# Kernel tuning notes

Measured on AMD Instinct MI355X. Metric: run time of the kernel, lower is better.

## Reference

```python
import jax, jax.numpy as jnp
import numpy as np

TAU = 2.0          # LIF membrane time constant (decay_input=True)
VTH = 1.0          # spiking threshold (hidden layers); last layer has inf threshold
EPS = 1e-5         # batchnorm eps
ALPHA = 2.0        # ATan surrogate-gradient alpha
HL = 8             # HLfreq_ratio (chunk length in timesteps)
SIZES = [1024, 1024, 512]

@jax.custom_vjp
def spike(x):
    return (x >= 0).astype(x.dtype)

def _spike_fwd(x):
    return (x >= 0).astype(x.dtype), x

def _spike_bwd(x, g):
    # spikingjelly ATan surrogate: alpha/2 / (1 + (pi/2 * alpha * x)^2)
    return (g * (ALPHA / 2.0) / (1.0 + (jnp.pi / 2.0 * ALPHA * x) ** 2),)

spike.defvjp(_spike_fwd, _spike_bwd)

def setup_inputs() -> dict:
    key = jax.random.key(0)
    ks = jax.random.split(key, 1 + len(SIZES))
    T, B, D = 1024, 32, 512
    inp = {"x": jax.random.normal(ks[0], (T, B, D), dtype=jnp.float32)}
    d_in = D
    for i, s in enumerate(SIZES):
        inp[f"W{i}"] = jax.random.normal(ks[i + 1], (s, d_in), dtype=jnp.float32) / np.float32(np.sqrt(d_in))
        inp[f"b{i}"] = jnp.zeros((s,), jnp.float32)
        inp[f"g{i}"] = jnp.ones((s,), jnp.float32)    # BN gamma
        inp[f"bt{i}"] = jnp.zeros((s,), jnp.float32)  # BN beta
        d_in = s
    return inp

def _forward(x, params):
    # x: [T, B, d_in]; process chunks of HL timesteps, membrane state carried across chunks
    n_chunks = x.shape[0] // HL
    B = x.shape[1]
    xr = x.reshape(n_chunks, HL, B, x.shape[2])
    n_layers = len(params)
    vs0 = tuple(jnp.zeros((B, p[0].shape[0]), x.dtype) for p in params)

    def chunk_step(vs, xc):  # xc: [HL, B, d_in]
        h = xc
        new_vs = []
        for i, (W, b, g, bt) in enumerate(params):
            # Linear over all timesteps of the chunk
            h = jnp.einsum('tbd,ed->tbe', h, W) + b
            # BatchNorm (training mode): stats over (time, batch) of this chunk, per channel
            mu = h.mean((0, 1))
            var = jnp.mean((h - mu) ** 2, (0, 1))
            h = g * (h - mu) * jax.lax.rsqrt(var + EPS) + bt
            last = (i == n_layers - 1)

            def step(v, xt, last=last):
                v = v + (xt - v) / TAU          # decay_input=True LIF charge
                if last:
                    return v, v                 # inf threshold: pure leaky integrator, emit v_seq
                s = spike(v - VTH)
                return v * (1.0 - s), s         # hard reset to v_reset=0

            v_new, h = jax.lax.scan(step, vs[i], h)
            new_vs.append(v_new)
        # reduction_mode='mean_mempot': mean of last layer's v_seq over chunk timesteps
        return tuple(new_vs), h.mean(0)

    _, z = jax.lax.scan(chunk_step, vs0, xr)
    return z  # [n_chunks, B, d_output]

def reference(x, W0, b0, g0, bt0, W1, b1, g1, bt1, W2, b2, g2, bt2):
    params = [(W0, b0, g0, bt0), (W1, b1, g1, bt1), (W2, b2, g2, bt2)]
    return _forward(x, params)
```

## Files before the change

kernel.cpp:

```cpp
#include <hip/hip_runtime.h>
#include <hip/hip_bf16.h>
#include <stdint.h>


__global__ void k_zero(unsigned int* __restrict__ p, int n){
  int i = blockIdx.x * 256 + threadIdx.x;
  if (i < n) p[i] = 0u;
}

__global__ void k_transpose(const float* __restrict__ in, float* __restrict__ out, int R, int C){
  __shared__ float tile[32][33];
  int bx = blockIdx.x * 32, by = blockIdx.y * 32;
  int tx = threadIdx.x, ty = threadIdx.y;
  for (int i = ty; i < 32; i += 8)
    tile[i][tx] = in[(size_t)(by + i) * C + bx + tx];
  __syncthreads();
  for (int i = ty; i < 32; i += 8)
    out[(size_t)(bx + i) * R + by + tx] = tile[tx][i];
}

__global__ __launch_bounds__(256, 3) void k_gemm_np(const float* __restrict__ A,
    const float* __restrict__ Bw, const float* __restrict__ bias,
    float* __restrict__ C, int M){
  (void)M;
  __shared__ float As[32][132];
  __shared__ float Bs[32][132];
  int bm = blockIdx.y * 128;
  int bn = blockIdx.x * 128;
  int tid = threadIdx.x;
  int kk = tid & 31, q = tid >> 5;
  int c = (tid & 7) | ((tid & 64) >> 3);
  int r = ((tid >> 3) & 7) | ((tid & 128) >> 4);
  int giA = (2 * r) ^ (r >> 2);
  int giB = (2 * c) ^ (c >> 2);
  float acc[8][8];
#pragma unroll
  for (int ii = 0; ii < 8; ++ii)
#pragma unroll
    for (int jj = 0; jj < 8; ++jj) acc[ii][jj] = 0.f;

  for (int k0 = 0; k0 < 512; k0 += 32){
#pragma unroll
    for (int rr = 0; rr < 4; ++rr){
      int colb = q * 4 + rr * 32;
      int gi = (colb >> 2) ^ (colb >> 5) ^ (kk >> 3);
      float4 va, vb;
      va.x = A[(size_t)(bm + colb + 0) * 512 + k0 + kk];
      va.y = A[(size_t)(bm + colb + 1) * 512 + k0 + kk];
      va.z = A[(size_t)(bm + colb + 2) * 512 + k0 + kk];
      va.w = A[(size_t)(bm + colb + 3) * 512 + k0 + kk];
      vb.x = Bw[(size_t)(bn + colb + 0) * 512 + k0 + kk];
      vb.y = Bw[(size_t)(bn + colb + 1) * 512 + k0 + kk];
      vb.z = Bw[(size_t)(bn + colb + 2) * 512 + k0 + kk];
      vb.w = Bw[(size_t)(bn + colb + 3) * 512 + k0 + kk];
      *(float4*)&As[kk][gi << 2] = va;
      *(float4*)&Bs[kk][gi << 2] = vb;
    }
    __syncthreads();
#pragma unroll
    for (int kg = 0; kg < 4; ++kg){
      const int sa = (giA ^ kg) << 2;
      const int sb = (giB ^ kg) << 2;
#pragma unroll
      for (int k8 = 0; k8 < 8; ++k8){
        const int k = kg * 8 + k8;
        float4 av0 = *(const float4*)&As[k][sa];
        float4 av1 = *(const float4*)&As[k][sa ^ 4];
        float4 bv0 = *(const float4*)&Bs[k][sb];
        float4 bv1 = *(const float4*)&Bs[k][sb ^ 4];
        float a[8] = {av0.x, av0.y, av0.z, av0.w, av1.x, av1.y, av1.z, av1.w};
        float b[8] = {bv0.x, bv0.y, bv0.z, bv0.w, bv1.x, bv1.y, bv1.z, bv1.w};
#pragma unroll
        for (int ii = 0; ii < 8; ++ii)
#pragma unroll
          for (int jj = 0; jj < 8; ++jj)
            acc[ii][jj] = __fmaf_rn(a[ii], b[jj], acc[ii][jj]);
      }
    }
    __syncthreads();
  }

  float* S = &As[0][0];
  float4 bi0 = *(const float4*)(bias + bn + c * 8);
  float4 bi1 = *(const float4*)(bias + bn + c * 8 + 4);
  int rrow = tid >> 3;
  int f    = tid & 7;
  size_t mr = (size_t)(bm + (rrow >> 1) * 8 + (rrow & 1));
#pragma unroll
  for (int t4 = 0; t4 < 4; ++t4){
#pragma unroll
    for (int p = 0; p < 2; ++p){
      const int ii = t4 * 2 + p;
      const int row = r * 2 + p;
      const int giW = (2 * c) ^ (c >> 2) ^ (row >> 3);
      float4 o0, o1;
      o0.x = __fadd_rn(acc[ii][0], bi0.x);
      o0.y = __fadd_rn(acc[ii][1], bi0.y);
      o0.z = __fadd_rn(acc[ii][2], bi0.z);
      o0.w = __fadd_rn(acc[ii][3], bi0.w);
      o1.x = __fadd_rn(acc[ii][4], bi1.x);
      o1.y = __fadd_rn(acc[ii][5], bi1.y);
      o1.z = __fadd_rn(acc[ii][6], bi1.z);
      o1.w = __fadd_rn(acc[ii][7], bi1.w);
      *(float4*)&S[row * 132 + (giW << 2)] = o0;
      *(float4*)&S[row * 132 + ((giW << 2) ^ 4)] = o1;
    }
    __syncthreads();
#pragma unroll
    for (int u = 0; u < 4; ++u){
      int col4 = 4 * f + 32 * u;
      int giR = (f + 8 * u) ^ u ^ (rrow >> 3);
      float4 v = *(const float4*)&S[rrow * 132 + (giR << 2)];
      *(float4*)&C[(mr + (size_t)t4 * 2) * 1024 + bn + col4] = v;
    }
    __syncthreads();
  }
}

__global__ __launch_bounds__(256) void k_stats_np(const float* __restrict__ A,
    float* __restrict__ mu, float* __restrict__ var, int Dch, int c0){
  int cl = blockIdx.x;
  int ch = blockIdx.y * 256 + threadIdx.x;
  const float* base = A + (size_t)cl * 256 * Dch + ch;
  float acc = 0.f;
  for (int s = 0; s < 256; ++s)
    acc = __fadd_rn(acc, base[(size_t)s * Dch]);
  float m = __fmul_rn(acc, 1.f / 256.f);
  float vacc = 0.f;
  for (int s = 0; s < 256; ++s){
    float d = __fsub_rn(base[(size_t)s * Dch], m);
    vacc = __fadd_rn(vacc, __fmul_rn(d, d));
  }
  int c = c0 + cl;
  mu[(size_t)c * Dch + ch]  = m;
  var[(size_t)c * Dch + ch] = __fmul_rn(vacc, 1.f / 256.f);
}

__global__ __launch_bounds__(64) void k_scan_spike_np(const float* __restrict__ A,
    const float* __restrict__ mu, const float* __restrict__ var,
    const float* __restrict__ g, const float* __restrict__ bt,
    float* __restrict__ vstate, unsigned long long* __restrict__ mask,
    int Dch, int c0, int nb){
  int ebn = Dch >> 6;
  int eb = blockIdx.x % ebn;
  int b  = blockIdx.x / ebn;
  int e  = (eb << 6) + threadIdx.x;
  float gg = g[e], bb = bt[e];
  float v = vstate[(size_t)b * Dch + e];
  float hbuf[8];
#pragma unroll
  for (int t = 0; t < 8; ++t)
    hbuf[t] = A[(size_t)(t * 32 + b) * Dch + e];
  for (int cl = 0; cl < nb; ++cl){
    int c = c0 + cl;
    float m  = mu[(size_t)c * Dch + e];
    float ve = __fadd_rn(var[(size_t)c * Dch + e], 1e-5f);
    float sq = (float)sqrt((double)ve);
    float r  = (float)(1.0 / (double)sq);
    float hn[8];
    if (cl + 1 < nb){
#pragma unroll
      for (int t = 0; t < 8; ++t)
        hn[t] = A[(size_t)(((cl + 1) * 8 + t) * 32 + b) * Dch + e];
    } else {
#pragma unroll
      for (int t = 0; t < 8; ++t) hn[t] = 0.f;
    }
#pragma unroll
    for (int t = 0; t < 8; ++t){
      int sl = (cl * 8 + t) * 32 + b;
      float xn = __fadd_rn(__fmul_rn(__fmul_rn(gg, __fsub_rn(hbuf[t], m)), r), bb);
      v = __fadd_rn(v, __fmul_rn(__fsub_rn(xn, v), 0.5f));
      bool sp = (v >= 1.0f);
      unsigned long long bal = __ballot(sp);
      if (sp) v = 0.0f;
      if (threadIdx.x == 0) mask[(size_t)sl * 16 + eb] = bal;
    }
#pragma unroll
    for (int t = 0; t < 8; ++t) hbuf[t] = hn[t];
  }
  vstate[(size_t)b * Dch + e] = v;
}

__global__ __launch_bounds__(256) void k_sparse_np(const unsigned long long* __restrict__ mask,
    const float* __restrict__ WT, const float* __restrict__ bias,
    float* __restrict__ C, int Dout){
  int tid = threadIdx.x;
  int lane = tid & 63;
  int wid = tid >> 6;
  int wps = Dout >> 8;
  int chgrp = wid % wps;
  int sgrp  = wid / wps;
  int spb   = 4 / wps;
  int s = blockIdx.x * spb + sgrp;
  int ch = (chgrp << 8) + (lane << 2);
  __shared__ unsigned short list[2][1024];
  __shared__ int nlist[2];

  if (chgrp == 0 && lane < 16){
    unsigned long long mw = mask[(size_t)s * 16 + lane];
    int cnt = __popcll(mw);
    int base = 0;
#pragma unroll
    for (int w = 0; w < 16; ++w){
      int cw = __shfl(cnt, w, 64);
      base += (w < lane) ? cw : 0;
    }
    int idx = base;
    while (mw){
      int bit = __ffsll(mw) - 1;
      mw &= mw - 1;
      list[sgrp][idx++] = (unsigned short)((lane << 6) + bit);
    }
    if (lane == 15) nlist[sgrp] = base + cnt;
  }
  __syncthreads();
  int n = nlist[sgrp];
  const unsigned short* il = list[sgrp];
  float a0 = 0.f, a1 = 0.f, a2 = 0.f, a3 = 0.f;
  int i = 0;
  for (; i + 8 <= n; i += 8){
    float4 wv[8];
#pragma unroll
    for (int u = 0; u < 8; ++u)
      wv[u] = *(const float4*)(WT + (size_t)il[i + u] * Dout + ch);
#pragma unroll
    for (int u = 0; u < 8; ++u){
      a0 = __fadd_rn(a0, wv[u].x); a1 = __fadd_rn(a1, wv[u].y);
      a2 = __fadd_rn(a2, wv[u].z); a3 = __fadd_rn(a3, wv[u].w);
    }
  }
  for (; i < n; ++i){
    int d = il[i];
    float4 wv = *(const float4*)(WT + (size_t)d * Dout + ch);
    a0 = __fadd_rn(a0, wv.x); a1 = __fadd_rn(a1, wv.y); a2 = __fadd_rn(a2, wv.z); a3 = __fadd_rn(a3, wv.w);
  }
  float4 bb = *(const float4*)(bias + ch);
  float4 o;
  o.x = __fadd_rn(a0, bb.x);
  o.y = __fadd_rn(a1, bb.y);
  o.z = __fadd_rn(a2, bb.z);
  o.w = __fadd_rn(a3, bb.w);
  *(float4*)(C + (size_t)s * Dout + ch) = o;
}

__global__ __launch_bounds__(64) void k_scan_last_np(const float* __restrict__ A,
    const float* __restrict__ mu, const float* __restrict__ var,
    const float* __restrict__ g, const float* __restrict__ bt,
    float* __restrict__ vstate, float* __restrict__ out, int c0, int nb){
  const int Dch = 512;
  int eb = blockIdx.x & 7;
  int b  = blockIdx.x >> 3;
  int e  = (eb << 6) + threadIdx.x;
  float gg = g[e], bb = bt[e];
  float v = vstate[(size_t)b * Dch + e];
  float hbuf[8];
#pragma unroll
  for (int t = 0; t < 8; ++t)
    hbuf[t] = A[(size_t)(t * 32 + b) * Dch + e];
  for (int cl = 0; cl < nb; ++cl){
    int c = c0 + cl;
    float m  = mu[(size_t)c * Dch + e];
    float ve = __fadd_rn(var[(size_t)c * Dch + e], 1e-5f);
    float sq = (float)sqrt((double)ve);
    float r  = (float)(1.0 / (double)sq);
    float hn[8];
    if (cl + 1 < nb){
#pragma unroll
      for (int t = 0; t < 8; ++t)
        hn[t] = A[(size_t)(((cl + 1) * 8 + t) * 32 + b) * Dch + e];
    } else {
#pragma unroll
      for (int t = 0; t < 8; ++t) hn[t] = 0.f;
    }
    float macc = 0.f;
#pragma unroll
    for (int t = 0; t < 8; ++t){
      float xn = __fadd_rn(__fmul_rn(__fmul_rn(gg, __fsub_rn(hbuf[t], m)), r), bb);
      v = __fadd_rn(v, __fmul_rn(__fsub_rn(xn, v), 0.5f));
      macc = __fadd_rn(macc, v);
    }
    out[((size_t)c * 32 + b) * 512 + e] = __fmul_rn(macc, 0.125f);
#pragma unroll
    for (int t = 0; t < 8; ++t) hbuf[t] = hn[t];
  }
  vstate[(size_t)b * Dch + e] = v;
}

static inline size_t al256(size_t x){ return (x + 255) & ~(size_t)255; }

extern "C" void kernel_launch(void* const* d_in, const int* in_sizes, int n_in,
                              void* d_out, int out_size, void* d_ws, size_t ws_size,
                              hipStream_t stream){
  (void)in_sizes; (void)n_in; (void)out_size;
  const float* x   = (const float*)d_in[0];
  const float* W0  = (const float*)d_in[1];
  const float* b0  = (const float*)d_in[2];
  const float* g0  = (const float*)d_in[3];
  const float* bt0 = (const float*)d_in[4];
  const float* W1  = (const float*)d_in[5];
  const float* b1  = (const float*)d_in[6];
  const float* g1  = (const float*)d_in[7];
  const float* bt1 = (const float*)d_in[8];
  const float* W2  = (const float*)d_in[9];
  const float* b2  = (const float*)d_in[10];
  const float* g2  = (const float*)d_in[11];
  const float* bt2 = (const float*)d_in[12];
  float* out = (float*)d_out;

  char* p = (char*)d_ws;
  auto carve = [&](size_t bytes)->char*{ char* q = p; p += al256(bytes); return q; };
  float* W1T  = (float*)carve((size_t)1024 * 1024 * 4);
  float* W2T  = (float*)carve((size_t)1024 * 512 * 4);
  float* mu0  = (float*)carve((size_t)128 * 1024 * 4);
  float* var0 = (float*)carve((size_t)128 * 1024 * 4);
  float* mu1  = (float*)carve((size_t)128 * 1024 * 4);
  float* var1 = (float*)carve((size_t)128 * 1024 * 4);
  float* mu2  = (float*)carve((size_t)128 * 512 * 4);
  float* var2 = (float*)carve((size_t)128 * 512 * 4);
  float* v0   = (float*)carve((size_t)32 * 1024 * 4);
  float* v1   = (float*)carve((size_t)32 * 1024 * 4);
  float* v2   = (float*)carve((size_t)32 * 512 * 4);
  size_t fixed_used = (size_t)(p - (char*)d_ws);

  auto need = [&](int nb)->size_t{
    return al256((size_t)nb * 256 * 1024 * 4)
         + 2 * al256((size_t)nb * 256 * 16 * 8);
  };
  int NB = 128;
  while (NB > 1 && fixed_used + need(NB) > ws_size) NB >>= 1;
  if (fixed_used + need(NB) > ws_size) return;

  float*              a_buf = (float*)carve((size_t)NB * 256 * 1024 * 4);
  unsigned long long* mask0 = (unsigned long long*)carve((size_t)NB * 256 * 16 * 8);
  unsigned long long* mask1 = (unsigned long long*)carve((size_t)NB * 256 * 16 * 8);

  {
    int nz = 32 * (1024 + 1024 + 512);
    k_zero<<<dim3((nz + 255) / 256), dim3(256), 0, stream>>>((unsigned int*)v0, nz);
  }
  k_transpose<<<dim3(32, 32), dim3(32, 8), 0, stream>>>(W1, W1T, 1024, 1024);
  k_transpose<<<dim3(32, 16), dim3(32, 8), 0, stream>>>(W2, W2T, 512, 1024);

  int nblk = 128 / NB;
  for (int cb = 0; cb < nblk; ++cb){
    int c0 = cb * NB;
    int M = NB * 256;
    const float* xblk = x + (size_t)c0 * 256 * 512;

    k_gemm_np<<<dim3(8, M / 128), dim3(256), 0, stream>>>(xblk, W0, b0, a_buf, M);
    k_stats_np<<<dim3(NB, 4), dim3(256), 0, stream>>>(a_buf, mu0, var0, 1024, c0);
    k_scan_spike_np<<<dim3(32 * 16), dim3(64), 0, stream>>>(a_buf, mu0, var0, g0, bt0, v0, mask0, 1024, c0, NB);

    k_sparse_np<<<dim3(M), dim3(256), 0, stream>>>(mask0, W1T, b1, a_buf, 1024);
    k_stats_np<<<dim3(NB, 4), dim3(256), 0, stream>>>(a_buf, mu1, var1, 1024, c0);
    k_scan_spike_np<<<dim3(32 * 16), dim3(64), 0, stream>>>(a_buf, mu1, var1, g1, bt1, v1, mask1, 1024, c0, NB);

    k_sparse_np<<<dim3(M / 2), dim3(256), 0, stream>>>(mask1, W2T, b2, a_buf, 512);
    k_stats_np<<<dim3(NB, 2), dim3(256), 0, stream>>>(a_buf, mu2, var2, 512, c0);
    k_scan_last_np<<<dim3(32 * 8), dim3(64), 0, stream>>>(a_buf, mu2, var2, g2, bt2, v2, out, c0, NB);
  }
}
```

Before: 1.112 ms.

## Batch 32 rows per block in sparse spike-weight accumulation to reuse weight loads

Replaces the per-row sparse gather kernel with one where each thread group handles all 32 batch rows of a timestep. The spike masks are transposed in shared memory into per-input 32-bit batch masks, so each weight row is loaded once and added into up to 32 register accumulators. The aim is to cut repeated global weight reads across batch rows. In exchange it streams every weight row whether or not any row spiked, holds 128 float accumulators per thread (high register pressure), and launches far fewer blocks.

Measured after the change: 2.712 ms. 144% more time.

```diff
diff --git a/kernel.cpp b/kernel.cpp
--- a/kernel.cpp
+++ b/kernel.cpp
@@ -182,66 +182,83 @@
   vstate[(size_t)b * Dch + e] = v;
 }
 
-__global__ __launch_bounds__(256) void k_sparse_np(const unsigned long long* __restrict__ mask,
+template<int DOUT>
+__global__ __launch_bounds__(256, 2) void k_sparse_grp(
+    const unsigned long long* __restrict__ mask,
     const float* __restrict__ WT, const float* __restrict__ bias,
-    float* __restrict__ C, int Dout){
-  int tid = threadIdx.x;
-  int lane = tid & 63;
-  int wid = tid >> 6;
-  int wps = Dout >> 8;
-  int chgrp = wid % wps;
-  int sgrp  = wid / wps;
-  int spb   = 4 / wps;
-  int s = blockIdx.x * spb + sgrp;
-  int ch = (chgrp << 8) + (lane << 2);
-  __shared__ unsigned short list[2][1024];
-  __shared__ int nlist[2];
-
-  if (chgrp == 0 && lane < 16){
-    unsigned long long mw = mask[(size_t)s * 16 + lane];
-    int cnt = __popcll(mw);
-    int base = 0;
-#pragma unroll
-    for (int w = 0; w < 16; ++w){
-      int cw = __shfl(cnt, w, 64);
-      base += (w < lane) ? cw : 0;
-    }
-    int idx = base;
-    while (mw){
-      int bit = __ffsll(mw) - 1;
-      mw &= mw - 1;
-      list[sgrp][idx++] = (unsigned short)((lane << 6) + bit);
-    }
-    if (lane == 15) nlist[sgrp] = base + cnt;
-  }
+    float* __restrict__ C){
+  constexpr int GPB = 1024 / DOUT;
+  constexpr int TPG = 256 / GPB;
+  const int tid  = threadIdx.x;
+  const int grp  = tid / TPG;
+  const int gtid = tid % TPG;
+  const int t    = blockIdx.x * GPB + grp;
+  const int ch   = gtid * 4;
+
+  __shared__ unsigned long long mk[GPB][32][16];
+  __shared__ unsigned int m32s[GPB][1024];
+
+  for (int i = gtid; i < 512; i += TPG)
+    mk[grp][i >> 4][i & 15] = mask[(size_t)(t * 32 + (i >> 4)) * 16 + (i & 15)];
   __syncthreads();
-  int n = nlist[sgrp];
-  const unsigned short* il = list[sgrp];
-  float a0 = 0.f, a1 = 0.f, a2 = 0.f, a3 = 0.f;
-  int i = 0;
-  for (; i + 8 <= n; i += 8){
-    float4 wv[8];
-#pragma unroll
-    for (int u = 0; u < 8; ++u)
-      wv[u] = *(const float4*)(WT + (size_t)il[i + u] * Dout + ch);
-#pragma unroll
-    for (int u = 0; u < 8; ++u){
-      a0 = __fadd_rn(a0, wv[u].x); a1 = __fadd_rn(a1, wv[u].y);
-      a2 = __fadd_rn(a2, wv[u].z); a3 = __fadd_rn(a3, wv[u].w);
-    }
-  }
-  for (; i < n; ++i){
-    int d = il[i];
-    float4 wv = *(const float4*)(WT + (size_t)d * Dout + ch);
-    a0 = __fadd_rn(a0, wv.x); a1 = __fadd_rn(a1, wv.y); a2 = __fadd_rn(a2, wv.z); a3 = __fadd_rn(a3, wv.w);
-  }
-  float4 bb = *(const float4*)(bias + ch);
-  float4 o;
-  o.x = __fadd_rn(a0, bb.x);
-  o.y = __fadd_rn(a1, bb.y);
-  o.z = __fadd_rn(a2, bb.z);
-  o.w = __fadd_rn(a3, bb.w);
-  *(float4*)(C + (size_t)s * Dout + ch) = o;
+
+  for (int d0 = gtid * 4; d0 < 1024; d0 += TPG * 4){
+    unsigned int v0 = 0, v1 = 0, v2 = 0, v3 = 0;
+    const int wi = d0 >> 6, sh = d0 & 63;
+#pragma unroll
+    for (int b = 0; b < 32; ++b){
+      unsigned int nib = (unsigned int)((mk[grp][b][wi] >> sh) & 0xfull);
+      v0 |= (nib & 1u) << b;
+      v1 |= ((nib >> 1) & 1u) << b;
+      v2 |= ((nib >> 2) & 1u) << b;
+      v3 |= ((nib >> 3) & 1u) << b;
+    }
+    m32s[grp][d0 + 0] = v0;
+    m32s[grp][d0 + 1] = v1;
+    m32s[grp][d0 + 2] = v2;
+    m32s[grp][d0 + 3] = v3;
+  }
+  __syncthreads();
+
+  float4 acc[32];
+#pragma unroll
+  for (int b = 0; b < 32; ++b) acc[b] = make_float4(0.f, 0.f, 0.f, 0.f);
+
+  const float* __restrict__ Wc = WT + ch;
+  unsigned int m0 = __builtin_amdgcn_readfirstlane(m32s[grp][0]);
+  unsigned int m1 = __builtin_amdgcn_readfirstlane(m32s[grp][1]);
+  float4 w0 = *(const float4*)(Wc);
+  float4 w1 = *(const float4*)(Wc + DOUT);
+  for (int d = 0; d < 1024; ++d){
+    const unsigned int m = m0;
+    const float4 w = w0;
+    m0 = m1; w0 = w1;
+    if (d + 2 < 1024){
+      m1 = __builtin_amdgcn_readfirstlane(m32s[grp][d + 2]);
+      w1 = *(const float4*)(Wc + (size_t)(d + 2) * DOUT);
+    }
+    if (!m) continue;
+#pragma unroll
+    for (int b = 0; b < 32; ++b){
+      if (m & (1u << b)){
+        acc[b].x = __fadd_rn(acc[b].x, w.x);
+        acc[b].y = __fadd_rn(acc[b].y, w.y);
+        acc[b].z = __fadd_rn(acc[b].z, w.z);
+        acc[b].w = __fadd_rn(acc[b].w, w.w);
+      }
+    }
+  }
+
+  const float4 bb4 = *(const float4*)(bias + ch);
+#pragma unroll
+  for (int b = 0; b < 32; ++b){
+    float4 o;
+    o.x = __fadd_rn(acc[b].x, bb4.x);
+    o.y = __fadd_rn(acc[b].y, bb4.y);
+    o.z = __fadd_rn(acc[b].z, bb4.z);
+    o.w = __fadd_rn(acc[b].w, bb4.w);
+    *(float4*)&C[(size_t)(t * 32 + b) * DOUT + ch] = o;
+  }
 }
 
 __global__ __launch_bounds__(64) void k_scan_last_np(const float* __restrict__ A,
@@ -352,11 +369,11 @@
     k_stats_np<<<dim3(NB, 4), dim3(256), 0, stream>>>(a_buf, mu0, var0, 1024, c0);
     k_scan_spike_np<<<dim3(32 * 16), dim3(64), 0, stream>>>(a_buf, mu0, var0, g0, bt0, v0, mask0, 1024, c0, NB);
 
-    k_sparse_np<<<dim3(M), dim3(256), 0, stream>>>(mask0, W1T, b1, a_buf, 1024);
+    k_sparse_grp<1024><<<dim3(M / 32), dim3(256), 0, stream>>>(mask0, W1T, b1, a_buf);
     k_stats_np<<<dim3(NB, 4), dim3(256), 0, stream>>>(a_buf, mu1, var1, 1024, c0);
     k_scan_spike_np<<<dim3(32 * 16), dim3(64), 0, stream>>>(a_buf, mu1, var1, g1, bt1, v1, mask1, 1024, c0, NB);
 
-    k_sparse_np<<<dim3(M / 2), dim3(256), 0, stream>>>(mask1, W2T, b2, a_buf, 512);
+    k_sparse_grp<512><<<dim3(M / 64), dim3(256), 0, stream>>>(mask1, W2T, b2, a_buf);
     k_stats_np<<<dim3(NB, 2), dim3(256), 0, stream>>>(a_buf, mu2, var2, 512, c0);
     k_scan_last_np<<<dim3(32 * 8), dim3(64), 0, stream>>>(a_buf, mu2, var2, g2, bt2, v2, out, c0, NB);
   }
```

## Enlarge layer-0 GEMM tile to 256x128 with 16x8 per-thread micro-tile

Applied to the files above, without the earlier changes.

The first-layer FP32 GEMM tile grows from 128x128 to 256x128 rows per block, so each thread accumulates a 16x8 micro-tile instead of 8x8. This raises FMA work per shared-memory load and reuses each W tile across more rows. In exchange register pressure rises (occupancy hint drops from 3 to 2 blocks), the grid has half as many blocks, and the epilogue is rewritten to stage 64-row slices through LDS.

Result: slower. 1.157 ms (+4.1%).

```diff
diff --git a/kernel.cpp b/kernel.cpp
--- a/kernel.cpp
+++ b/kernel.cpp
@@ -19,59 +19,69 @@
     out[(size_t)(bx + i) * R + by + tx] = tile[tx][i];
 }
 
-__global__ __launch_bounds__(256, 3) void k_gemm_np(const float* __restrict__ A,
+__global__ __launch_bounds__(256, 2) void k_gemm_np(const float* __restrict__ A,
     const float* __restrict__ Bw, const float* __restrict__ bias,
     float* __restrict__ C, int M){
   (void)M;
-  __shared__ float As[32][132];
-  __shared__ float Bs[32][132];
-  int bm = blockIdx.y * 128;
+  __shared__ float LDS[32 * 260 + 32 * 132];
+  float* As = LDS;
+  float* Bs = LDS + 32 * 260;
+  int bm = blockIdx.y * 256;
   int bn = blockIdx.x * 128;
   int tid = threadIdx.x;
   int kk = tid & 31, q = tid >> 5;
   int c = (tid & 7) | ((tid & 64) >> 3);
   int r = ((tid >> 3) & 7) | ((tid & 128) >> 4);
-  int giA = (2 * r) ^ (r >> 2);
-  int giB = (2 * c) ^ (c >> 2);
-  float acc[8][8];
-#pragma unroll
-  for (int ii = 0; ii < 8; ++ii)
+  int gA = (4 * r) ^ (r >> 1);
+  int gB = (2 * c) ^ (c >> 2);
+  float acc[16][8];
+#pragma unroll
+  for (int ii = 0; ii < 16; ++ii)
 #pragma unroll
     for (int jj = 0; jj < 8; ++jj) acc[ii][jj] = 0.f;
 
   for (int k0 = 0; k0 < 512; k0 += 32){
 #pragma unroll
-    for (int rr = 0; rr < 4; ++rr){
+    for (int rr = 0; rr < 8; ++rr){
       int colb = q * 4 + rr * 32;
       int gi = (colb >> 2) ^ (colb >> 5) ^ (kk >> 3);
-      float4 va, vb;
+      float4 va;
       va.x = A[(size_t)(bm + colb + 0) * 512 + k0 + kk];
       va.y = A[(size_t)(bm + colb + 1) * 512 + k0 + kk];
       va.z = A[(size_t)(bm + colb + 2) * 512 + k0 + kk];
       va.w = A[(size_t)(bm + colb + 3) * 512 + k0 + kk];
+      *(float4*)&As[kk * 260 + (gi << 2)] = va;
+    }
+#pragma unroll
+    for (int rr = 0; rr < 4; ++rr){
+      int colb = q * 4 + rr * 32;
+      int gi = (colb >> 2) ^ (colb >> 5) ^ (kk >> 3);
+      float4 vb;
       vb.x = Bw[(size_t)(bn + colb + 0) * 512 + k0 + kk];
       vb.y = Bw[(size_t)(bn + colb + 1) * 512 + k0 + kk];
       vb.z = Bw[(size_t)(bn + colb + 2) * 512 + k0 + kk];
       vb.w = Bw[(size_t)(bn + colb + 3) * 512 + k0 + kk];
-      *(float4*)&As[kk][gi << 2] = va;
-      *(float4*)&Bs[kk][gi << 2] = vb;
+      *(float4*)&Bs[kk * 132 + (gi << 2)] = vb;
     }
     __syncthreads();
 #pragma unroll
     for (int kg = 0; kg < 4; ++kg){
-      const int sa = (giA ^ kg) << 2;
-      const int sb = (giB ^ kg) << 2;
+      const int sa = (gA ^ kg) << 2;
+      const int sb = (gB ^ kg) << 2;
 #pragma unroll
       for (int k8 = 0; k8 < 8; ++k8){
         const int k = kg * 8 + k8;
-        float4 av0 = *(const float4*)&As[k][sa];
-        float4 av1 = *(const float4*)&As[k][sa ^ 4];
-        float4 bv0 = *(const float4*)&Bs[k][sb];
-        float4 bv1 = *(const float4*)&Bs[k][sb ^ 4];
-        float a[8] = {av0.x, av0.y, av0.z, av0.w, av1.x, av1.y, av1.z, av1.w};
-        float b[8] = {bv0.x, bv0.y, bv0.z, bv0.w, bv1.x, bv1.y, bv1.z, bv1.w};
-#pragma unroll
-        for (int ii = 0; ii < 8; ++ii)
+        float4 av0 = *(const float4*)&As[k * 260 + sa];
+        float4 av1 = *(const float4*)&As[k * 260 + (sa ^ 4)];
+        float4 av2 = *(const float4*)&As[k * 260 + (sa ^ 8)];
+        float4 av3 = *(const float4*)&As[k * 260 + (sa ^ 12)];
+        float4 bv0 = *(const float4*)&Bs[k * 132 + sb];
+        float4 bv1 = *(const float4*)&Bs[k * 132 + (sb ^ 4)];
+        float a[16] = {av0.x, av0.y, av0.z, av0.w, av1.x, av1.y, av1.z, av1.w,
+                       av2.x, av2.y, av2.z, av2.w, av3.x, av3.y, av3.z, av3.w};
+        float b[8]  = {bv0.x, bv0.y, bv0.z, bv0.w, bv1.x, bv1.y, bv1.z, bv1.w};
+#pragma unroll
+        for (int ii = 0; ii < 16; ++ii)
 #pragma unroll
           for (int jj = 0; jj < 8; ++jj)
             acc[ii][jj] = __fmaf_rn(a[ii], b[jj], acc[ii][jj]);
@@ -80,38 +90,35 @@
     __syncthreads();
   }
 
-  float* S = &As[0][0];
   float4 bi0 = *(const float4*)(bias + bn + c * 8);
   float4 bi1 = *(const float4*)(bias + bn + c * 8 + 4);
-  int rrow = tid >> 3;
-  int f    = tid & 7;
-  size_t mr = (size_t)(bm + (rrow >> 1) * 8 + (rrow & 1));
-#pragma unroll
-  for (int t4 = 0; t4 < 4; ++t4){
-#pragma unroll
-    for (int p = 0; p < 2; ++p){
-      const int ii = t4 * 2 + p;
-      const int row = r * 2 + p;
-      const int giW = (2 * c) ^ (c >> 2) ^ (row >> 3);
-      float4 o0, o1;
-      o0.x = __fadd_rn(acc[ii][0], bi0.x);
-      o0.y = __fadd_rn(acc[ii][1], bi0.y);
-      o0.z = __fadd_rn(acc[ii][2], bi0.z);
-      o0.w = __fadd_rn(acc[ii][3], bi0.w);
-      o1.x = __fadd_rn(acc[ii][4], bi1.x);
-      o1.y = __fadd_rn(acc[ii][5], bi1.y);
-      o1.z = __fadd_rn(acc[ii][6], bi1.z);
-      o1.w = __fadd_rn(acc[ii][7], bi1.w);
-      *(float4*)&S[row * 132 + (giW << 2)] = o0;
-      *(float4*)&S[row * 132 + ((giW << 2) ^ 4)] = o1;
+#pragma unroll
+  for (int t = 0; t < 4; ++t){
+    if ((r >> 2) == t){
+#pragma unroll
+      for (int ii = 0; ii < 16; ++ii){
+        const int lr = (r & 3) * 16 + ii;
+        float4 o0, o1;
+        o0.x = __fadd_rn(acc[ii][0], bi0.x);
+        o0.y = __fadd_rn(acc[ii][1], bi0.y);
+        o0.z = __fadd_rn(acc[ii][2], bi0.z);
+        o0.w = __fadd_rn(acc[ii][3], bi0.w);
+        o1.x = __fadd_rn(acc[ii][4], bi1.x);
+        o1.y = __fadd_rn(acc[ii][5], bi1.y);
+        o1.z = __fadd_rn(acc[ii][6], bi1.z);
+        o1.w = __fadd_rn(acc[ii][7], bi1.w);
+        *(float4*)&LDS[lr * 132 + c * 8]     = o0;
+        *(float4*)&LDS[lr * 132 + c * 8 + 4] = o1;
+      }
     }
     __syncthreads();
 #pragma unroll
-    for (int u = 0; u < 4; ++u){
-      int col4 = 4 * f + 32 * u;
-      int giR = (f + 8 * u) ^ u ^ (rrow >> 3);
-      float4 v = *(const float4*)&S[rrow * 132 + (giR << 2)];
-      *(float4*)&C[(mr + (size_t)t4 * 2) * 1024 + bn + col4] = v;
+    for (int u = 0; u < 8; ++u){
+      int idx = u * 256 + tid;
+      int row = idx >> 5;
+      int ch4 = (idx & 31) << 2;
+      float4 v = *(const float4*)&LDS[row * 132 + ch4];
+      *(float4*)&C[(size_t)(bm + t * 64 + row) * 1024 + bn + ch4] = v;
     }
     __syncthreads();
   }
@@ -348,7 +355,7 @@
     int M = NB * 256;
     const float* xblk = x + (size_t)c0 * 256 * 512;
 
-    k_gemm_np<<<dim3(8, M / 128), dim3(256), 0, stream>>>(xblk, W0, b0, a_buf, M);
+    k_gemm_np<<<dim3(8, M / 256), dim3(256), 0, stream>>>(xblk, W0, b0, a_buf, M);
     k_stats_np<<<dim3(NB, 4), dim3(256), 0, stream>>>(a_buf, mu0, var0, 1024, c0);
     k_scan_spike_np<<<dim3(32 * 16), dim3(64), 0, stream>>>(a_buf, mu0, var0, g0, bt0, v0, mask0, 1024, c0, NB);
 
```
